# Performance work log

Hardware: AMD Instinct MI355X
Metric: run time of the kernel (lower is better)

Reference implementation:

```python
import jax, jax.numpy as jnp
import numpy as np

E = 1_000_000      # number of edges
N_NODE = 200_000   # nodes in this layer's frontier
IN_DIM = 64
ATTN_DIM = 64
OUT_DIM = 64
N_REL = 200
N_ENT = 50_000
B = 8              # batchsize


def setup_inputs() -> dict:
    key = jax.random.key(0)
    ks = jax.random.split(key, 16)
    # edges columns: [r_idx, _, rel, _, sub, obj]
    r_idx = jax.random.randint(ks[0], (E,), 0, B)
    rel = jax.random.randint(ks[1], (E,), 0, 2 * N_REL + 1)
    sub = jax.random.randint(ks[2], (E,), 0, N_NODE)
    obj = jax.random.randint(ks[3], (E,), 0, N_NODE)
    zeros = jnp.zeros((E,), dtype=jnp.int64 if jax.config.jax_enable_x64 else jnp.int32)
    edges = jnp.stack([r_idx, zeros, rel, zeros, sub, obj], axis=1)

    q_sub = jax.random.randint(ks[4], (B,), 0, N_ENT)
    q_rel = jax.random.randint(ks[5], (B,), 0, 2 * N_REL + 1)
    hidden = jax.random.normal(ks[6], (N_NODE, IN_DIM), dtype=jnp.float32)
    nodes = jnp.stack([jax.random.randint(ks[7], (N_NODE,), 0, B),
                       jax.random.randint(ks[8], (N_NODE,), 0, N_ENT)], axis=1)
    old_nodes_new_idx = jnp.sort(jax.random.randint(ks[9], (N_NODE // 2,), 0, N_NODE))

    s = 1.0 / np.sqrt(IN_DIM)
    rela_embed = jax.random.normal(ks[10], (2 * N_REL + 1, IN_DIM), dtype=jnp.float32)
    Ws = jax.random.uniform(ks[11], (ATTN_DIM, IN_DIM), minval=-s, maxval=s)  # Ws_attn.weight
    Wr = jax.random.uniform(ks[12], (ATTN_DIM, IN_DIM), minval=-s, maxval=s)  # Wr_attn.weight
    Wqr_W = jax.random.uniform(ks[13], (ATTN_DIM, IN_DIM), minval=-s, maxval=s)
    Wqr_b = jax.random.uniform(ks[14], (ATTN_DIM,), minval=-s, maxval=s)
    sa = 1.0 / np.sqrt(ATTN_DIM)
    kk = jax.random.split(ks[15], 3)
    wa_W = jax.random.uniform(kk[0], (1, ATTN_DIM), minval=-sa, maxval=sa)  # w_alpha.weight
    wa_b = jax.random.uniform(kk[1], (1,), minval=-sa, maxval=sa)
    Wh = jax.random.uniform(kk[2], (OUT_DIM, IN_DIM), minval=-s, maxval=s)  # W_h.weight

    return {"q_sub": q_sub, "q_rel": q_rel, "hidden": hidden, "edges": edges,
            "nodes": nodes, "old_nodes_new_idx": old_nodes_new_idx, "batchsize": B,
            "rela_embed": rela_embed, "Ws": Ws, "Wr": Wr, "Wqr_W": Wqr_W,
            "Wqr_b": Wqr_b, "wa_W": wa_W, "wa_b": wa_b, "Wh": Wh}


def reference(q_sub, q_rel, hidden, edges, nodes, old_nodes_new_idx, batchsize,
              rela_embed, Ws, Wr, Wqr_W, Wqr_b, wa_W, wa_b, Wh):
    sub = edges[:, 4]
    rel = edges[:, 2]
    obj = edges[:, 5]
    r_idx = edges[:, 0]
    n_node = nodes.shape[0]

    hs = hidden[sub]                      # [E, in_dim] gather
    hr = rela_embed[rel]                  # [E, in_dim]
    h_qr = rela_embed[q_rel][r_idx]       # [E, in_dim]

    # attention MLP: relu(Ws hs + Wr hr + Wqr h_qr + b) -> scalar -> sigmoid gate
    attn_input = (jnp.einsum('ei,ai->ea', hs, Ws)
                  + jnp.einsum('ei,ai->ea', hr, Wr)
                  + jnp.einsum('ei,ai->ea', h_qr, Wqr_W) + Wqr_b)  # [E, attn_dim]
    alpha = jax.nn.sigmoid(jax.nn.relu(attn_input) @ wa_W.T + wa_b)  # [E, 1]

    message = alpha * (hs + hr)                                       # [E, in_dim]
    message_agg = jax.ops.segment_sum(message, obj, num_segments=n_node)  # [n_node, in_dim]
    hidden_new = message_agg @ Wh.T  # act is identity (default)
    return hidden_new
```

## Files before the change

### kernel.cpp

```cpp
#include <hip/hip_runtime.h>
#include <hip/hip_bf16.h>


__global__ __launch_bounds__(256) void rowproj64(const float* src,
                                                 const float* __restrict__ W,
                                                 float* dst, int nrows) {
    __shared__ float Wt[64][65];
    __shared__ float4 Sl[64][16];
    int tid = threadIdx.x;
    for (int i = tid; i < 4096; i += 256) Wt[i & 63][i >> 6] = W[i];
    long r0 = (long)blockIdx.x * 64;
    const float4* src4 = (const float4*)(src + r0 * 64);
    float4* s4 = (float4*)Sl;
    for (int i = tid; i < 1024; i += 256) s4[i] = src4[i];
    __syncthreads();
    int c = tid & 63;
    int rbase = (tid >> 6) * 16;
    float w[64];
#pragma unroll
    for (int k = 0; k < 64; ++k) w[k] = Wt[k][c];
#pragma unroll
    for (int r = 0; r < 16; ++r) {
        float a0 = 0.f, a1 = 0.f, a2 = 0.f, a3 = 0.f;
#pragma unroll
        for (int k4 = 0; k4 < 16; ++k4) {
            float4 s = Sl[rbase + r][k4];
            a0 += s.x * w[4 * k4 + 0];
            a1 += s.y * w[4 * k4 + 1];
            a2 += s.z * w[4 * k4 + 2];
            a3 += s.w * w[4 * k4 + 3];
        }
        dst[(r0 + rbase + r) * 64 + c] = (a0 + a1) + (a2 + a3);
    }
}

__global__ void k_ct(const float* __restrict__ rela,
                     const int* __restrict__ q_rel,
                     const float* __restrict__ Wr,
                     const float* __restrict__ Wqr,
                     const float* __restrict__ bqr,
                     float* __restrict__ ct, int B) {
    int rel = blockIdx.x, a = threadIdx.x;
    __shared__ float hr[64];
    __shared__ float hq[8][64];
    hr[a] = rela[(size_t)rel * 64 + a];
    for (int b = 0; b < B; ++b) hq[b][a] = rela[(size_t)q_rel[b] * 64 + a];
    __syncthreads();
    float accr = 0.f;
#pragma unroll
    for (int k = 0; k < 64; ++k) accr += hr[k] * Wr[a * 64 + k];
    for (int b = 0; b < B; ++b) {
        float acc = bqr[a];
#pragma unroll
        for (int k = 0; k < 64; ++k) acc += hq[b][k] * Wqr[a * 64 + k];
        ct[((size_t)rel * 8 + b) * 64 + a] = accr + acc;
    }
}

__global__ void k_count(const int* __restrict__ edges, int E,
                        int* __restrict__ deg) {
    int e = blockIdx.x * blockDim.x + threadIdx.x;
    if (e < E) atomicAdd(&deg[edges[(size_t)e * 6 + 5]], 1);
}

#define SCAN_BS 256
__global__ __launch_bounds__(SCAN_BS) void k_scan_block(
    const int* __restrict__ deg, int N,
    int* __restrict__ rowptr, int* __restrict__ bsum) {
    __shared__ int sh[SCAN_BS];
    int t = threadIdx.x, b = blockIdx.x;
    int base = b * 1024 + t * 4;
    int d0 = (base + 0 < N) ? deg[base + 0] : 0;
    int d1 = (base + 1 < N) ? deg[base + 1] : 0;
    int d2 = (base + 2 < N) ? deg[base + 2] : 0;
    int d3 = (base + 3 < N) ? deg[base + 3] : 0;
    int s = d0 + d1 + d2 + d3;
    sh[t] = s;
    __syncthreads();
    for (int o = 1; o < SCAN_BS; o <<= 1) {
        int v = (t >= o) ? sh[t - o] : 0;
        __syncthreads();
        sh[t] += v;
        __syncthreads();
    }
    int run = sh[t] - s;
    if (t == SCAN_BS - 1) bsum[b] = sh[t];
    if (base + 0 < N) rowptr[base + 0] = run;  run += d0;
    if (base + 1 < N) rowptr[base + 1] = run;  run += d1;
    if (base + 2 < N) rowptr[base + 2] = run;  run += d2;
    if (base + 3 < N) rowptr[base + 3] = run;
}

__global__ __launch_bounds__(SCAN_BS) void k_scan_partials(
    const int* __restrict__ bsum, int* __restrict__ boffs, int NB) {
    __shared__ int sh[SCAN_BS];
    int t = threadIdx.x;
    int v = (t < NB) ? bsum[t] : 0;
    sh[t] = v;
    __syncthreads();
    for (int o = 1; o < SCAN_BS; o <<= 1) {
        int u = (t >= o) ? sh[t - o] : 0;
        __syncthreads();
        sh[t] += u;
        __syncthreads();
    }
    if (t < NB) boffs[t] = sh[t] - v;
}

__global__ void k_add_offsets(int* __restrict__ rowptr,
                              int* __restrict__ cursor,
                              const int* __restrict__ boffs, int N, int E) {
    int i = blockIdx.x * blockDim.x + threadIdx.x;
    if (i < N) {
        int v = rowptr[i] + boffs[i >> 10];
        rowptr[i] = v;
        cursor[i] = v;
    }
    if (i == 0) rowptr[N] = E;
}

__global__ void k_key(const int* __restrict__ edges, int E,
                      int* __restrict__ cursor,
                      unsigned int* __restrict__ key) {
    int e = blockIdx.x * blockDim.x + threadIdx.x;
    if (e >= E) return;
    const int* ed = edges + (size_t)e * 6;
    int r_idx = ed[0], rel = ed[2], sub = ed[4], obj = ed[5];
    int pos = atomicAdd(&cursor[obj], 1);
    key[pos] = (unsigned int)sub | ((unsigned int)(rel * 8 + r_idx) << 18);
}

__global__ __launch_bounds__(256) void k_agg(
    const int* __restrict__ rowptr,
    const unsigned int* __restrict__ key,
    const float* __restrict__ hproj,
    const float* __restrict__ ct,
    const float* __restrict__ hidden,
    const float* __restrict__ rela,
    const float* __restrict__ wa,
    const float* __restrict__ wab_p,
    float* __restrict__ agg, int N) {
    int lane = threadIdx.x & 63;
    int w = (int)((blockIdx.x * blockDim.x + threadIdx.x) >> 6);
    if (w >= N) return;
    int n = __builtin_amdgcn_readfirstlane(w);
    int s = rowptr[n], e = rowptr[n + 1];
    float wav = wa[lane];
    float wab = wab_p[0];
    float acc = 0.f;
    if (s < e) {
        unsigned int k0 = key[s];
        int sub = (int)(k0 & 0x3FFFFu);
        int cr  = (int)(k0 >> 18);
        float hp = hproj[(size_t)sub * 64 + lane];
        float cv = ct[(size_t)cr * 64 + lane];
        float hd = hidden[(size_t)sub * 64 + lane];
        float rl = rela[(size_t)(cr >> 3) * 64 + lane];
        for (int j = s + 1; j < e; ++j) {
            unsigned int k1 = key[j];
            int sub1 = (int)(k1 & 0x3FFFFu);
            int cr1  = (int)(k1 >> 18);
            float hp1 = hproj[(size_t)sub1 * 64 + lane];
            float cv1 = ct[(size_t)cr1 * 64 + lane];
            float hd1 = hidden[(size_t)sub1 * 64 + lane];
            float rl1 = rela[(size_t)(cr1 >> 3) * 64 + lane];
            float t = fmaxf(hp + cv, 0.f) * wav;
#pragma unroll
            for (int o = 32; o; o >>= 1) t += __shfl_xor(t, o, 64);
            float alpha = 1.f / (1.f + __expf(-(t + wab)));
            acc += alpha * (hd + rl);
            hp = hp1; cv = cv1; hd = hd1; rl = rl1;
        }
        float t = fmaxf(hp + cv, 0.f) * wav;
#pragma unroll
        for (int o = 32; o; o >>= 1) t += __shfl_xor(t, o, 64);
        float alpha = 1.f / (1.f + __expf(-(t + wab)));
        acc += alpha * (hd + rl);
    }
    agg[(size_t)n * 64 + lane] = acc;
}

extern "C" void kernel_launch(void* const* d_in, const int* in_sizes, int n_in,
                              void* d_out, int out_size, void* d_ws, size_t ws_size,
                              hipStream_t stream) {
    const int* q_rel    = (const int*)d_in[1];
    const float* hidden = (const float*)d_in[2];
    const int* edges    = (const int*)d_in[3];
    const float* rela   = (const float*)d_in[7];
    const float* Ws     = (const float*)d_in[8];
    const float* Wr     = (const float*)d_in[9];
    const float* WqrW   = (const float*)d_in[10];
    const float* Wqrb   = (const float*)d_in[11];
    const float* waW    = (const float*)d_in[12];
    const float* wab    = (const float*)d_in[13];
    const float* Wh     = (const float*)d_in[14];

    int E = in_sizes[3] / 6;
    int n_node = in_sizes[4] / 2;
    int n_rel_tot = in_sizes[7] / 64;
    int B = in_sizes[0];
    int NB = (n_node + 1023) / 1024;

    float* agg = (float*)d_out;
    char* w = (char*)d_ws;
    float* hproj = (float*)w;                  w += (size_t)n_node * 64 * 4;
    float* ct    = (float*)w;                  w += (size_t)n_rel_tot * 8 * 64 * 4;
    unsigned int* key = (unsigned int*)w;      w += (size_t)E * 4;
    int* deg    = (int*)w;                     w += (size_t)n_node * 4;
    int* cursor = (int*)w;                     w += (size_t)n_node * 4;
    int* rowptr = (int*)w;                     w += (size_t)(n_node + 1) * 4;
    int* bsum   = (int*)w;                     w += (size_t)NB * 4;
    int* boffs  = (int*)w;                     w += (size_t)NB * 4;

    rowproj64<<<n_node / 64, 256, 0, stream>>>(hidden, Ws, hproj, n_node);
    k_ct<<<n_rel_tot, 64, 0, stream>>>(rela, q_rel, Wr, WqrW, Wqrb, ct, B);

    hipMemsetAsync(deg, 0, (size_t)n_node * 4, stream);
    k_count<<<(E + 255) / 256, 256, 0, stream>>>(edges, E, deg);
    k_scan_block<<<NB, SCAN_BS, 0, stream>>>(deg, n_node, rowptr, bsum);
    k_scan_partials<<<1, SCAN_BS, 0, stream>>>(bsum, boffs, NB);
    k_add_offsets<<<(n_node + 255) / 256, 256, 0, stream>>>(rowptr, cursor,
                                                            boffs, n_node, E);

    k_key<<<(E + 255) / 256, 256, 0, stream>>>(edges, E, cursor, key);
    k_agg<<<(n_node * 64 + 255) / 256, 256, 0, stream>>>(
        rowptr, key, hproj, ct, hidden, rela, waW, wab, agg, n_node);
    rowproj64<<<n_node / 64, 256, 0, stream>>>(agg, Wh, agg, n_node);
}
```

Baseline: 448.4 us.

## Record edge rank in count pass and process two edges per wave in aggregation

The count kernel now stores the atomic return value as each edge's rank within its destination bucket. The scatter kernel then computes the position from rowptr plus rank instead of running a second atomic pass over a cursor array. The aggregation kernel splits each 64-lane wave into two halves that handle alternate edges with float2 loads, reduces over 32 lanes, and combines the halves at the end. This doubles the edges in flight per wave and removes the atomic scatter, at the cost of an extra E-sized rank buffer and masking for odd degree counts.

```diff
diff --git a/kernel.cpp b/kernel.cpp
--- a/kernel.cpp
+++ b/kernel.cpp
@@ -58,9 +58,9 @@
 }
 
 __global__ void k_count(const int* __restrict__ edges, int E,
-                        int* __restrict__ deg) {
+                        int* __restrict__ deg, int* __restrict__ rank) {
     int e = blockIdx.x * blockDim.x + threadIdx.x;
-    if (e < E) atomicAdd(&deg[edges[(size_t)e * 6 + 5]], 1);
+    if (e < E) rank[e] = atomicAdd(&deg[edges[(size_t)e * 6 + 5]], 1);
 }
 
 #define SCAN_BS 256
@@ -108,25 +108,21 @@
 }
 
 __global__ void k_add_offsets(int* __restrict__ rowptr,
-                              int* __restrict__ cursor,
                               const int* __restrict__ boffs, int N, int E) {
     int i = blockIdx.x * blockDim.x + threadIdx.x;
-    if (i < N) {
-        int v = rowptr[i] + boffs[i >> 10];
-        rowptr[i] = v;
-        cursor[i] = v;
-    }
+    if (i < N) rowptr[i] += boffs[i >> 10];
     if (i == 0) rowptr[N] = E;
 }
 
 __global__ void k_key(const int* __restrict__ edges, int E,
-                      int* __restrict__ cursor,
+                      const int* __restrict__ rowptr,
+                      const int* __restrict__ rank,
                       unsigned int* __restrict__ key) {
     int e = blockIdx.x * blockDim.x + threadIdx.x;
     if (e >= E) return;
     const int* ed = edges + (size_t)e * 6;
     int r_idx = ed[0], rel = ed[2], sub = ed[4], obj = ed[5];
-    int pos = atomicAdd(&cursor[obj], 1);
+    int pos = rowptr[obj] + rank[e];
     key[pos] = (unsigned int)sub | ((unsigned int)(rel * 8 + r_idx) << 18);
 }
 
@@ -141,43 +137,63 @@
     const float* __restrict__ wab_p,
     float* __restrict__ agg, int N) {
     int lane = threadIdx.x & 63;
+    int half = lane >> 5;
+    int li   = lane & 31;
     int w = (int)((blockIdx.x * blockDim.x + threadIdx.x) >> 6);
     if (w >= N) return;
     int n = __builtin_amdgcn_readfirstlane(w);
     int s = rowptr[n], e = rowptr[n + 1];
-    float wav = wa[lane];
+    const float2* hproj2  = (const float2*)hproj;
+    const float2* ct2     = (const float2*)ct;
+    const float2* hidden2 = (const float2*)hidden;
+    const float2* rela2   = (const float2*)rela;
+    float2 wav = ((const float2*)wa)[li];
     float wab = wab_p[0];
-    float acc = 0.f;
+    float2 acc = {0.f, 0.f};
+
     if (s < e) {
-        unsigned int k0 = key[s];
-        int sub = (int)(k0 & 0x3FFFFu);
-        int cr  = (int)(k0 >> 18);
-        float hp = hproj[(size_t)sub * 64 + lane];
-        float cv = ct[(size_t)cr * 64 + lane];
-        float hd = hidden[(size_t)sub * 64 + lane];
-        float rl = rela[(size_t)(cr >> 3) * 64 + lane];
-        for (int j = s + 1; j < e; ++j) {
-            unsigned int k1 = key[j];
-            int sub1 = (int)(k1 & 0x3FFFFu);
-            int cr1  = (int)(k1 >> 18);
-            float hp1 = hproj[(size_t)sub1 * 64 + lane];
-            float cv1 = ct[(size_t)cr1 * 64 + lane];
-            float hd1 = hidden[(size_t)sub1 * 64 + lane];
-            float rl1 = rela[(size_t)(cr1 >> 3) * 64 + lane];
-            float t = fmaxf(hp + cv, 0.f) * wav;
-#pragma unroll
-            for (int o = 32; o; o >>= 1) t += __shfl_xor(t, o, 64);
-            float alpha = 1.f / (1.f + __expf(-(t + wab)));
-            acc += alpha * (hd + rl);
-            hp = hp1; cv = cv1; hd = hd1; rl = rl1;
+        int j1c = min(s + 1, e - 1);
+        unsigned int ka = key[s], kb = key[j1c];
+        unsigned int kk = half ? kb : ka;
+        float vld = (half == 0 || s + 1 < e) ? 1.f : 0.f;
+        int sub = (int)(kk & 0x3FFFFu);
+        int cr  = (int)(kk >> 18);
+        float2 hp = hproj2[(size_t)sub * 32 + li];
+        float2 cv = ct2[(size_t)cr * 32 + li];
+        float2 hd = hidden2[(size_t)sub * 32 + li];
+        float2 rl = rela2[(size_t)(cr >> 3) * 32 + li];
+
+        for (int j = s + 2; j < e; j += 2) {
+            int j1n = min(j + 1, e - 1);
+            unsigned int ka1 = key[j], kb1 = key[j1n];
+            unsigned int kk1 = half ? kb1 : ka1;
+            float vld1 = (half == 0 || j + 1 < e) ? 1.f : 0.f;
+            int sub1 = (int)(kk1 & 0x3FFFFu);
+            int cr1  = (int)(kk1 >> 18);
+            float2 hp1 = hproj2[(size_t)sub1 * 32 + li];
+            float2 cv1 = ct2[(size_t)cr1 * 32 + li];
+            float2 hd1 = hidden2[(size_t)sub1 * 32 + li];
+            float2 rl1 = rela2[(size_t)(cr1 >> 3) * 32 + li];
+            float t = fmaxf(hp.x + cv.x, 0.f) * wav.x
+                    + fmaxf(hp.y + cv.y, 0.f) * wav.y;
+#pragma unroll
+            for (int o = 16; o; o >>= 1) t += __shfl_xor(t, o, 64);
+            float am = vld / (1.f + __expf(-(t + wab)));
+            acc.x += am * (hd.x + rl.x);
+            acc.y += am * (hd.y + rl.y);
+            hp = hp1; cv = cv1; hd = hd1; rl = rl1; vld = vld1;
         }
-        float t = fmaxf(hp + cv, 0.f) * wav;
-#pragma unroll
-        for (int o = 32; o; o >>= 1) t += __shfl_xor(t, o, 64);
-        float alpha = 1.f / (1.f + __expf(-(t + wab)));
-        acc += alpha * (hd + rl);
-    }
-    agg[(size_t)n * 64 + lane] = acc;
+        float t = fmaxf(hp.x + cv.x, 0.f) * wav.x
+                + fmaxf(hp.y + cv.y, 0.f) * wav.y;
+#pragma unroll
+        for (int o = 16; o; o >>= 1) t += __shfl_xor(t, o, 64);
+        float am = vld / (1.f + __expf(-(t + wab)));
+        acc.x += am * (hd.x + rl.x);
+        acc.y += am * (hd.y + rl.y);
+    }
+    acc.x += __shfl_xor(acc.x, 32, 64);
+    acc.y += __shfl_xor(acc.y, 32, 64);
+    if (half == 0) ((float2*)agg)[(size_t)n * 32 + li] = acc;
 }
 
 extern "C" void kernel_launch(void* const* d_in, const int* in_sizes, int n_in,
@@ -206,8 +222,8 @@
     float* hproj = (float*)w;                  w += (size_t)n_node * 64 * 4;
     float* ct    = (float*)w;                  w += (size_t)n_rel_tot * 8 * 64 * 4;
     unsigned int* key = (unsigned int*)w;      w += (size_t)E * 4;
+    int* rank   = (int*)w;                     w += (size_t)E * 4;
     int* deg    = (int*)w;                     w += (size_t)n_node * 4;
-    int* cursor = (int*)w;                     w += (size_t)n_node * 4;
     int* rowptr = (int*)w;                     w += (size_t)(n_node + 1) * 4;
     int* bsum   = (int*)w;                     w += (size_t)NB * 4;
     int* boffs  = (int*)w;                     w += (size_t)NB * 4;
@@ -216,13 +232,13 @@
     k_ct<<<n_rel_tot, 64, 0, stream>>>(rela, q_rel, Wr, WqrW, Wqrb, ct, B);
 
     hipMemsetAsync(deg, 0, (size_t)n_node * 4, stream);
-    k_count<<<(E + 255) / 256, 256, 0, stream>>>(edges, E, deg);
+    k_count<<<(E + 255) / 256, 256, 0, stream>>>(edges, E, deg, rank);
     k_scan_block<<<NB, SCAN_BS, 0, stream>>>(deg, n_node, rowptr, bsum);
     k_scan_partials<<<1, SCAN_BS, 0, stream>>>(bsum, boffs, NB);
-    k_add_offsets<<<(n_node + 255) / 256, 256, 0, stream>>>(rowptr, cursor,
-                                                            boffs, n_node, E);
-
-    k_key<<<(E + 255) / 256, 256, 0, stream>>>(edges, E, cursor, key);
+    k_add_offsets<<<(n_node + 255) / 256, 256, 0, stream>>>(rowptr, boffs,
+                                                            n_node, E);
+
+    k_key<<<(E + 255) / 256, 256, 0, stream>>>(edges, E, rowptr, rank, key);
     k_agg<<<(n_node * 64 + 255) / 256, 256, 0, stream>>>(
         rowptr, key, hproj, ct, hidden, rela, waW, wab, agg, n_node);
     rowproj64<<<n_node / 64, 256, 0, stream>>>(agg, Wh, agg, n_node);
```

New measurement: 401.7 us. 10.4% less time.
